# Optimization experiments

Hardware: AMD Instinct MI355X
Metric: run time of the kernel (lower is better)

Reference implementation:

```python
import jax, jax.numpy as jnp
import numpy as np

B, N, PATCH_DIM, HIDDEN, POS_SIZE = 16, 4096, 768, 768, 10240


def setup_inputs() -> dict:
    key = jax.random.key(0)
    k1, k2, k3, k4, k5 = jax.random.split(key, 5)
    pixel_values = jax.random.uniform(k1, (B, N, PATCH_DIM), dtype=jnp.float32)
    pixel_position_ids = jax.random.randint(k2, (B, N, 2), 0, POS_SIZE, dtype=jnp.int32)
    padding_mask = jax.random.randint(k3, (B, N), 0, 2).astype(bool)
    W_proj = jax.random.normal(k4, (HIDDEN, PATCH_DIM), dtype=jnp.float32) * 0.02
    pos_table = jax.random.normal(k5, (2, POS_SIZE, HIDDEN), dtype=jnp.float32) * 0.02
    return {
        "pixel_values": pixel_values,
        "pixel_position_ids": pixel_position_ids,
        "padding_mask": padding_mask,
        "W_proj": W_proj,
        "pos_table": pos_table,
    }


def reference(pixel_values, pixel_position_ids, padding_mask, W_proj, pos_table):
    # Rescale pixels to [-1, 1]
    x = 2.0 * (pixel_values - 0.5)
    # Linear(patch_dim -> hidden), bias=False: h = x @ W^T  -> [B, N, H]
    h = jnp.einsum("bnp,hp->bnh", x, W_proj)
    # Position embedding lookup. Original uses one_hot @ table; mathematically
    # identical to a direct gather per axis followed by a sum over the 2 axes.
    pos = jnp.clip(pixel_position_ids, 0, None)  # [B, N, 2]
    pe = pos_table[0][pos[..., 0]] + pos_table[1][pos[..., 1]]  # [B, N, H]
    pe = jnp.where(padding_mask[..., None], 0.0, pe)
    h = h + pe
    # masked_fill padded positions with 0
    h = jnp.where(padding_mask[..., None], 0.0, h)
    return h
```

## Files before the change

### kernel.cpp

```cpp
#include <hip/hip_runtime.h>
#include <hip/hip_bf16.h>

typedef __bf16 bf16_t;
typedef bf16_t bf16x4 __attribute__((ext_vector_type(4)));
typedef bf16_t bf16x8 __attribute__((ext_vector_type(8)));
typedef float f32x4 __attribute__((ext_vector_type(4)));

constexpr int NB   = 16;
constexpr int NN   = 4096;
constexpr int PD   = 768;
constexpr int HID  = 768;
constexpr int PSZ  = 10240;
constexpr int MT   = NB * NN;
constexpr int BM   = 128;
constexpr int BN   = 128;
constexpr int BK   = 32;
constexpr int NT   = PD / BK;
constexpr int LDSC = 132;
constexpr size_t PVN = (size_t)MT * PD;
constexpr size_t WN  = (size_t)HID * PD;

__device__ __forceinline__ bf16x8 cvt8_affine(const float4& x, const float4& y,
                                              float s, float o) {
    bf16x8 r;
    r[0] = (bf16_t)__builtin_fmaf(s, x.x, o);
    r[1] = (bf16_t)__builtin_fmaf(s, x.y, o);
    r[2] = (bf16_t)__builtin_fmaf(s, x.z, o);
    r[3] = (bf16_t)__builtin_fmaf(s, x.w, o);
    r[4] = (bf16_t)__builtin_fmaf(s, y.x, o);
    r[5] = (bf16_t)__builtin_fmaf(s, y.y, o);
    r[6] = (bf16_t)__builtin_fmaf(s, y.z, o);
    r[7] = (bf16_t)__builtin_fmaf(s, y.w, o);
    return r;
}

__device__ __forceinline__ bf16x4 cvt4_affine(const float4& x, float s, float o) {
    bf16x4 r;
    r[0] = (bf16_t)__builtin_fmaf(s, x.x, o);
    r[1] = (bf16_t)__builtin_fmaf(s, x.y, o);
    r[2] = (bf16_t)__builtin_fmaf(s, x.z, o);
    r[3] = (bf16_t)__builtin_fmaf(s, x.w, o);
    return r;
}

__global__ __launch_bounds__(256)
void compact_cvt(const float* __restrict__ pv,
                 const int* __restrict__ mask,
                 const float* __restrict__ W,
                 bf16_t* __restrict__ Ab,
                 bf16_t* __restrict__ Wb,
                 int* __restrict__ rowmap,
                 int* __restrict__ counter,
                 float* __restrict__ out)
{
    const int bid = blockIdx.x;
    const int tid = threadIdx.x;
    if (bid < 1024) {
        __shared__ int ls_slot[64];
        const int rowbase = bid * 64;
        const int lane = tid & 63;
        const int wv   = tid >> 6;
        if (wv == 0) {
            const int mk = mask[rowbase + lane];
            const unsigned long long b = __ballot(mk == 0);
            const int total = __popcll(b);
            const int pos = __popcll(b & ((1ull << lane) - 1ull));
            int gb = 0;
            if (lane == 0) gb = atomicAdd(counter, total);
            gb = __shfl(gb, 0);
            const int slot = (mk == 0) ? (gb + pos) : -1;
            ls_slot[lane] = slot;
            if (slot >= 0) rowmap[slot] = rowbase + lane;
        }
        __syncthreads();
        for (int i = wv; i < 64; i += 4) {
            const int slot = ls_slot[i];
            const int grow = rowbase + i;
            if (slot >= 0) {
                const float* src = pv + (size_t)grow * PD + lane * 12;
                bf16_t* dst = Ab + (size_t)slot * PD + lane * 12;
                #pragma unroll
                for (int q = 0; q < 3; ++q) {
                    const float4 v = *(const float4*)(src + q * 4);
                    *(bf16x4*)(dst + q * 4) = cvt4_affine(v, 2.f, -1.f);
                }
            } else {
                float* dst = out + (size_t)grow * HID + lane * 12;
                const float4 z{0.f, 0.f, 0.f, 0.f};
                #pragma unroll
                for (int q = 0; q < 3; ++q)
                    *(float4*)(dst + q * 4) = z;
            }
        }
    } else {
        const size_t nu = WN / 8;
        for (size_t u = (size_t)(bid - 1024) * 256 + tid; u < nu;
             u += (size_t)64 * 256) {
            const float4 x = ((const float4*)W)[2 * u];
            const float4 y = ((const float4*)W)[2 * u + 1];
            *(bf16x8*)(Wb + 8 * u) = cvt8_affine(x, y, 1.f, 0.f);
        }
    }
}

__global__ __launch_bounds__(256)
void cvt_kernel(const float* __restrict__ pv, const float* __restrict__ W,
                bf16_t* __restrict__ Ab, bf16_t* __restrict__ Wb)
{
    const size_t nunits = (PVN + WN) / 8;
    const size_t stride = (size_t)gridDim.x * blockDim.x;
    for (size_t u = (size_t)blockIdx.x * blockDim.x + threadIdx.x;
         u < nunits; u += stride) {
        if (u < PVN / 8) {
            const float4 x = ((const float4*)pv)[2 * u];
            const float4 y = ((const float4*)pv)[2 * u + 1];
            *(bf16x8*)(Ab + 8 * u) = cvt8_affine(x, y, 2.f, -1.f);
        } else {
            const size_t v = u - PVN / 8;
            const float4 x = ((const float4*)W)[2 * v];
            const float4 y = ((const float4*)W)[2 * v + 1];
            *(bf16x8*)(Wb + 8 * v) = cvt8_affine(x, y, 1.f, 0.f);
        }
    }
}

__device__ __forceinline__ void gload16(const void* g, void* l) {
    __builtin_amdgcn_global_load_lds(
        (const __attribute__((address_space(1))) void*)g,
        (__attribute__((address_space(3))) void*)l, 16, 0, 0);
}

template <bool USE_MAP>
__global__ __launch_bounds__(256, 2)
void gemm_kernel(const bf16_t* __restrict__ Ab,
                 const bf16_t* __restrict__ Wb,
                 const int* __restrict__ posids,
                 const int* __restrict__ mask,
                 const float* __restrict__ ptab,
                 float* __restrict__ out,
                 const int* __restrict__ rowmap,
                 const int* __restrict__ counter)
{
    __shared__ alignas(16) unsigned char smem[2 * (BM * BK + BN * BK) * 2];
    bf16_t* const Asb = (bf16_t*)smem;
    bf16_t* const Bsb = (bf16_t*)smem + 2 * BM * BK;
    float*  const Cs  = (float*)smem;

    int Mc = MT;
    int mt, nt;
    const int bid = blockIdx.x;
    if constexpr (USE_MAP) {
        Mc = counter[0];
        const int Mtiles = (Mc + BM - 1) / BM;
        const int nact = Mtiles * 6;
        if (bid >= nact) return;
        const int q = nact >> 3, rm = nact & 7;
        const int x = bid & 7, i = bid >> 3;
        const int logical = (x < rm ? x * (q + 1) : rm * (q + 1) + (x - rm) * q) + i;
        mt = logical / 6;
        nt = logical - mt * 6;
    } else {
        const int nwg = gridDim.x;
        const int cpx = nwg >> 3;
        const int logical = (bid & 7) * cpx + (bid >> 3);
        mt = logical / 6;
        nt = logical - mt * 6;
    }
    const int row0 = mt * BM;
    const int col0 = nt * BN;

    const int tid  = threadIdx.x;
    const int lane = tid & 63;
    const int wid  = tid >> 6;
    const int wm   = wid >> 1;
    const int wn   = wid & 1;

    const int srow = tid >> 2;
    const int sk   = (tid & 3) * 8;
    const bf16_t* a0 = Ab + (size_t)(row0 + srow) * PD + sk;
    const bf16_t* b0 = Wb + (size_t)(col0 + srow) * PD + sk;
    const int lds_lo = srow * BK + sk;
    const int lds_hi = (srow + 64) * BK + sk;

    f32x4 acc[4][4];
    #pragma unroll
    for (int i = 0; i < 4; ++i)
        #pragma unroll
        for (int j = 0; j < 4; ++j)
            acc[i][j] = f32x4{0.f, 0.f, 0.f, 0.f};

    const int lr = lane & 15;
    const int kg = lane >> 4;
    const int a_rd_off = (wm * 64 + lr) * BK + kg * 8;
    const int b_rd_off = (wn * 64 + lr) * BK + kg * 8;

    gload16(a0,           Asb + lds_lo);
    gload16(a0 + 64 * PD, Asb + lds_hi);
    gload16(b0,           Bsb + lds_lo);
    gload16(b0 + 64 * PD, Bsb + lds_hi);
    __syncthreads();

    int cur = 0;
    for (int t = 0; t < NT; ++t) {
        if (t + 1 < NT) {
            const int k1 = (t + 1) * BK;
            const int nb = cur ^ 1;
            gload16(a0 + k1,           Asb + nb * (BM * BK) + lds_lo);
            gload16(a0 + 64 * PD + k1, Asb + nb * (BM * BK) + lds_hi);
            gload16(b0 + k1,           Bsb + nb * (BN * BK) + lds_lo);
            gload16(b0 + 64 * PD + k1, Bsb + nb * (BN * BK) + lds_hi);
        }

        bf16x8 af[4], bfv[4];
        #pragma unroll
        for (int i = 0; i < 4; ++i) {
            af[i]  = *(const bf16x8*)(Asb + cur * (BM * BK) + a_rd_off + i * 16 * BK);
            bfv[i] = *(const bf16x8*)(Bsb + cur * (BN * BK) + b_rd_off + i * 16 * BK);
        }
        #pragma unroll
        for (int i = 0; i < 4; ++i)
            #pragma unroll
            for (int j = 0; j < 4; ++j)
                acc[i][j] = __builtin_amdgcn_mfma_f32_16x16x32_bf16(
                    af[i], bfv[j], acc[i][j], 0, 0, 0);

        __syncthreads();
        cur ^= 1;
    }

    const int lrow_w  = wm * 16 + kg * 4;
    const int lcol_w  = wn * 64 + lr;
    const int rr = tid >> 3;
    const int cg = tid & 7;
    const int erow_local = (rr & 15) + (rr >> 4) * 64;

    #pragma unroll
    for (int mi = 0; mi < 4; ++mi) {
        if (mi) __syncthreads();
        #pragma unroll
        for (int r = 0; r < 4; ++r)
            #pragma unroll
            for (int ni = 0; ni < 4; ++ni)
                Cs[(lrow_w + r) * LDSC + lcol_w + ni * 16] = acc[mi][ni][r];
        __syncthreads();

        const int crow = row0 + mi * 16 + erow_local;
        if constexpr (USE_MAP) {
            if (crow >= Mc) continue;
            const int grow = rowmap[crow];
            int p0 = posids[2 * grow];
            int p1 = posids[2 * grow + 1];
            p0 = p0 < 0 ? 0 : p0;
            p1 = p1 < 0 ? 0 : p1;
            const float* t0 = ptab + (size_t)p0 * HID + col0;
            const float* t1 = ptab + (size_t)PSZ * HID + (size_t)p1 * HID + col0;
            float* orow = out + (size_t)grow * HID + col0;
            #pragma unroll
            for (int j = 0; j < 4; ++j) {
                const int c = (cg + 8 * j) * 4;
                float4 v  = *(const float4*)&Cs[rr * LDSC + c];
                const float4 e0 = *(const float4*)(t0 + c);
                const float4 e1 = *(const float4*)(t1 + c);
                v.x += e0.x + e1.x;
                v.y += e0.y + e1.y;
                v.z += e0.z + e1.z;
                v.w += e0.w + e1.w;
                *(float4*)(orow + c) = v;
            }
        } else {
            const int grow = crow;
            float* orow = out + (size_t)grow * HID + col0;
            const int mk = mask[grow];
            if (mk) {
                const float4 z{0.f, 0.f, 0.f, 0.f};
                #pragma unroll
                for (int j = 0; j < 4; ++j)
                    *(float4*)(orow + (cg + 8 * j) * 4) = z;
            } else {
                int p0 = posids[2 * grow];
                int p1 = posids[2 * grow + 1];
                p0 = p0 < 0 ? 0 : p0;
                p1 = p1 < 0 ? 0 : p1;
                const float* t0 = ptab + (size_t)p0 * HID + col0;
                const float* t1 = ptab + (size_t)PSZ * HID + (size_t)p1 * HID + col0;
                #pragma unroll
                for (int j = 0; j < 4; ++j) {
                    const int c = (cg + 8 * j) * 4;
                    float4 v  = *(const float4*)&Cs[rr * LDSC + c];
                    const float4 e0 = *(const float4*)(t0 + c);
                    const float4 e1 = *(const float4*)(t1 + c);
                    v.x += e0.x + e1.x;
                    v.y += e0.y + e1.y;
                    v.z += e0.z + e1.z;
                    v.w += e0.w + e1.w;
                    *(float4*)(orow + c) = v;
                }
            }
        }
    }
}

constexpr int LDSS = 40;

__global__ __launch_bounds__(256, 2)
void vpe_kernel(const float* __restrict__ pv,
                const int* __restrict__ posids,
                const int* __restrict__ mask,
                const float* __restrict__ W,
                const float* __restrict__ ptab,
                float* __restrict__ out)
{
    __shared__ alignas(16) bf16_t As[2][BM * LDSS];
    __shared__ alignas(16) bf16_t Bs[2][BM * LDSS];

    const int nwg = gridDim.x;
    const int cpx = nwg >> 3;
    const int logical = (blockIdx.x & 7) * cpx + (blockIdx.x >> 3);
    const int mt = logical / 6;
    const int nt = logical - mt * 6;
    const int row0 = mt * BM;
    const int col0 = nt * BN;

    const int tid  = threadIdx.x;
    const int lane = tid & 63;
    const int wid  = tid >> 6;
    const int wm   = wid >> 1;
    const int wn   = wid & 1;
    const int srow = tid >> 1;
    const int scol = (tid & 1) << 4;

    const float* aptr = pv + (size_t)(row0 + srow) * PD + scol;
    const float* bptr = W  + (size_t)(col0 + srow) * PD + scol;
    const int lds_w_off = srow * LDSS + scol;

    f32x4 acc[4][4];
    #pragma unroll
    for (int i = 0; i < 4; ++i)
        #pragma unroll
        for (int j = 0; j < 4; ++j)
            acc[i][j] = f32x4{0.f, 0.f, 0.f, 0.f};

    const int lr = lane & 15;
    const int kg = lane >> 4;
    const int a_rd_off = (wm * 64 + lr) * LDSS + kg * 8;
    const int b_rd_off = (wn * 64 + lr) * LDSS + kg * 8;

    float4 ra[4], rb[4];
    #pragma unroll
    for (int q = 0; q < 4; ++q) {
        ra[q] = *(const float4*)(aptr + q * 4);
        rb[q] = *(const float4*)(bptr + q * 4);
    }
    {
        bf16x8 av0 = cvt8_affine(ra[0], ra[1], 2.f, -1.f);
        bf16x8 av1 = cvt8_affine(ra[2], ra[3], 2.f, -1.f);
        bf16x8 bv0 = cvt8_affine(rb[0], rb[1], 1.f, 0.f);
        bf16x8 bv1 = cvt8_affine(rb[2], rb[3], 1.f, 0.f);
        *(bf16x8*)(&As[0][lds_w_off])     = av0;
        *(bf16x8*)(&As[0][lds_w_off] + 8) = av1;
        *(bf16x8*)(&Bs[0][lds_w_off])     = bv0;
        *(bf16x8*)(&Bs[0][lds_w_off] + 8) = bv1;
    }
    __syncthreads();

    int cur = 0;
    for (int t = 0; t < NT - 1; ++t) {
        const int k1 = (t + 1) * BK;
        #pragma unroll
        for (int q = 0; q < 4; ++q) {
            ra[q] = *(const float4*)(aptr + k1 + q * 4);
            rb[q] = *(const float4*)(bptr + k1 + q * 4);
        }
        bf16x8 af[4], bfv[4];
        #pragma unroll
        for (int i = 0; i < 4; ++i) {
            af[i]  = *(const bf16x8*)(&As[cur][a_rd_off] + i * 16 * LDSS);
            bfv[i] = *(const bf16x8*)(&Bs[cur][b_rd_off] + i * 16 * LDSS);
        }
        #pragma unroll
        for (int i = 0; i < 4; ++i)
            #pragma unroll
            for (int j = 0; j < 4; ++j)
                acc[i][j] = __builtin_amdgcn_mfma_f32_16x16x32_bf16(
                    af[i], bfv[j], acc[i][j], 0, 0, 0);
        {
            bf16x8 av0 = cvt8_affine(ra[0], ra[1], 2.f, -1.f);
            bf16x8 av1 = cvt8_affine(ra[2], ra[3], 2.f, -1.f);
            bf16x8 bv0 = cvt8_affine(rb[0], rb[1], 1.f, 0.f);
            bf16x8 bv1 = cvt8_affine(rb[2], rb[3], 1.f, 0.f);
            const int nb = cur ^ 1;
            *(bf16x8*)(&As[nb][lds_w_off])     = av0;
            *(bf16x8*)(&As[nb][lds_w_off] + 8) = av1;
            *(bf16x8*)(&Bs[nb][lds_w_off])     = bv0;
            *(bf16x8*)(&Bs[nb][lds_w_off] + 8) = bv1;
        }
        __syncthreads();
        cur ^= 1;
    }
    {
        bf16x8 af[4], bfv[4];
        #pragma unroll
        for (int i = 0; i < 4; ++i) {
            af[i]  = *(const bf16x8*)(&As[cur][a_rd_off] + i * 16 * LDSS);
            bfv[i] = *(const bf16x8*)(&Bs[cur][b_rd_off] + i * 16 * LDSS);
        }
        #pragma unroll
        for (int i = 0; i < 4; ++i)
            #pragma unroll
            for (int j = 0; j < 4; ++j)
                acc[i][j] = __builtin_amdgcn_mfma_f32_16x16x32_bf16(
                    af[i], bfv[j], acc[i][j], 0, 0, 0);
    }
    #pragma unroll
    for (int mi = 0; mi < 4; ++mi) {
        #pragma unroll
        for (int r = 0; r < 4; ++r) {
            const int grow = row0 + wm * 64 + mi * 16 + kg * 4 + r;
            const int mk = mask[grow];
            int p0 = posids[2 * grow];
            int p1 = posids[2 * grow + 1];
            p0 = p0 < 0 ? 0 : p0;
            p1 = p1 < 0 ? 0 : p1;
            const float* t0 = ptab + (size_t)p0 * HID;
            const float* t1 = ptab + (size_t)PSZ * HID + (size_t)p1 * HID;
            float* orow = out + (size_t)grow * HID;
            #pragma unroll
            for (int ni = 0; ni < 4; ++ni) {
                const int col = col0 + wn * 64 + ni * 16 + lr;
                const float v = acc[mi][ni][r] + t0[col] + t1[col];
                orow[col] = mk ? 0.f : v;
            }
        }
    }
}

extern "C" void kernel_launch(void* const* d_in, const int* in_sizes, int n_in,
                              void* d_out, int out_size, void* d_ws, size_t ws_size,
                              hipStream_t stream) {
    (void)in_sizes; (void)n_in; (void)out_size;
    const float* pv     = (const float*)d_in[0];
    const int*   posids = (const int*)d_in[1];
    const int*   mask   = (const int*)d_in[2];
    const float* W      = (const float*)d_in[3];
    const float* ptab   = (const float*)d_in[4];
    float*       out    = (float*)d_out;

    const size_t AB_B = PVN * sizeof(bf16_t);
    const size_t WB_B = WN * sizeof(bf16_t);
    const size_t RM_B = (size_t)MT * 4;
    const size_t need1 = AB_B + WB_B;
    const size_t need2 = AB_B + WB_B + RM_B + 16;
    const int grid = (MT / BM) * (HID / BN);

    if (ws_size >= need2) {
        bf16_t* Ab   = (bf16_t*)d_ws;
        bf16_t* Wb   = Ab + PVN;
        int* rowmap  = (int*)((char*)d_ws + AB_B + WB_B);
        int* counter = (int*)((char*)d_ws + AB_B + WB_B + RM_B);
        hipMemsetAsync(counter, 0, 16, stream);
        hipLaunchKernelGGL(compact_cvt, dim3(1088), dim3(256), 0, stream,
                           pv, mask, W, Ab, Wb, rowmap, counter, out);
        hipLaunchKernelGGL((gemm_kernel<true>), dim3(grid), dim3(256), 0, stream,
                           Ab, Wb, posids, mask, ptab, out, rowmap, counter);
    } else if (ws_size >= need1) {
        bf16_t* Ab = (bf16_t*)d_ws;
        bf16_t* Wb = Ab + PVN;
        hipLaunchKernelGGL(cvt_kernel, dim3(2048), dim3(256), 0, stream,
                           pv, W, Ab, Wb);
        hipLaunchKernelGGL((gemm_kernel<false>), dim3(grid), dim3(256), 0, stream,
                           Ab, Wb, posids, mask, ptab, out, nullptr, nullptr);
    } else {
        hipLaunchKernelGGL(vpe_kernel, dim3(grid), dim3(256), 0, stream,
                           pv, posids, mask, W, ptab, out);
    }
}
```

Before: 167.6 us.

## Move masked-row zeroing into idle GEMM blocks and prefetch epilogue row indices

The compaction kernel now also records the indices of masked rows, stored from the end of rowmap, and no longer writes zeros to the output. GEMM blocks left idle by the compaction (beyond the active tile count) zero those masked output rows instead. This moves about half the output writes out of the conversion pass and overlaps them with the GEMM. The epilogue also loads each thread's rowmap and position ids for all four sub-tiles before the store loop, so that latency is not paid on every iteration. The cost is a second atomic per compaction block and a dependence on enough spare GEMM blocks existing.

```diff
diff --git a/kernel.cpp b/kernel.cpp
--- a/kernel.cpp
+++ b/kernel.cpp
@@ -50,8 +50,7 @@
                  bf16_t* __restrict__ Ab,
                  bf16_t* __restrict__ Wb,
                  int* __restrict__ rowmap,
-                 int* __restrict__ counter,
-                 float* __restrict__ out)
+                 int* __restrict__ counter)
 {
     const int bid = blockIdx.x;
     const int tid = threadIdx.x;
@@ -63,20 +62,32 @@
         if (wv == 0) {
             const int mk = mask[rowbase + lane];
             const unsigned long long b = __ballot(mk == 0);
+            const unsigned long long below = (1ull << lane) - 1ull;
             const int total = __popcll(b);
-            const int pos = __popcll(b & ((1ull << lane) - 1ull));
-            int gb = 0;
-            if (lane == 0) gb = atomicAdd(counter, total);
+            const int pos  = __popcll(b & below);
+            const int posm = __popcll(~b & below);
+            int gb = 0, gm = 0;
+            if (lane == 0) {
+                gb = atomicAdd(counter + 0, total);
+                gm = atomicAdd(counter + 1, 64 - total);
+            }
             gb = __shfl(gb, 0);
-            const int slot = (mk == 0) ? (gb + pos) : -1;
+            gm = __shfl(gm, 0);
+            int slot;
+            if (mk == 0) {
+                slot = gb + pos;
+                rowmap[slot] = rowbase + lane;
+            } else {
+                slot = -1;
+                rowmap[MT - 1 - (gm + posm)] = rowbase + lane;
+            }
             ls_slot[lane] = slot;
-            if (slot >= 0) rowmap[slot] = rowbase + lane;
         }
         __syncthreads();
         for (int i = wv; i < 64; i += 4) {
             const int slot = ls_slot[i];
-            const int grow = rowbase + i;
             if (slot >= 0) {
+                const int grow = rowbase + i;
                 const float* src = pv + (size_t)grow * PD + lane * 12;
                 bf16_t* dst = Ab + (size_t)slot * PD + lane * 12;
                 #pragma unroll
@@ -84,12 +95,6 @@
                     const float4 v = *(const float4*)(src + q * 4);
                     *(bf16x4*)(dst + q * 4) = cvt4_affine(v, 2.f, -1.f);
                 }
-            } else {
-                float* dst = out + (size_t)grow * HID + lane * 12;
-                const float4 z{0.f, 0.f, 0.f, 0.f};
-                #pragma unroll
-                for (int q = 0; q < 3; ++q)
-                    *(float4*)(dst + q * 4) = z;
             }
         }
     } else {
@@ -149,11 +154,27 @@
     int Mc = MT;
     int mt, nt;
     const int bid = blockIdx.x;
+    const int tid  = threadIdx.x;
+    const int lane = tid & 63;
+    const int wid  = tid >> 6;
     if constexpr (USE_MAP) {
         Mc = counter[0];
         const int Mtiles = (Mc + BM - 1) / BM;
         const int nact = Mtiles * 6;
-        if (bid >= nact) return;
+        if (bid >= nact) {
+            const int nspare = (int)gridDim.x - nact;
+            const int Mm = MT - Mc;
+            const int s = bid - nact;
+            const float4 z{0.f, 0.f, 0.f, 0.f};
+            for (int k = 4 * s + wid; k < Mm; k += 4 * nspare) {
+                const int grow = rowmap[MT - 1 - k];
+                float* dst = out + (size_t)grow * HID + lane * 12;
+                #pragma unroll
+                for (int q = 0; q < 3; ++q)
+                    *(float4*)(dst + q * 4) = z;
+            }
+            return;
+        }
         const int q = nact >> 3, rm = nact & 7;
         const int x = bid & 7, i = bid >> 3;
         const int logical = (x < rm ? x * (q + 1) : rm * (q + 1) + (x - rm) * q) + i;
@@ -169,9 +190,6 @@
     const int row0 = mt * BM;
     const int col0 = nt * BN;
 
-    const int tid  = threadIdx.x;
-    const int lane = tid & 63;
-    const int wid  = tid >> 6;
     const int wm   = wid >> 1;
     const int wn   = wid & 1;
 
@@ -234,6 +252,22 @@
     const int cg = tid & 7;
     const int erow_local = (rr & 15) + (rr >> 4) * 64;
 
+    int grow4[4], p04[4], p14[4];
+    #pragma unroll
+    for (int mi = 0; mi < 4; ++mi) {
+        int crow = row0 + mi * 16 + erow_local;
+        if constexpr (USE_MAP) {
+            const int cc = crow < Mc ? crow : Mc - 1;
+            grow4[mi] = rowmap[cc];
+        } else {
+            grow4[mi] = crow;
+        }
+        int p0 = posids[2 * grow4[mi]];
+        int p1 = posids[2 * grow4[mi] + 1];
+        p04[mi] = p0 < 0 ? 0 : p0;
+        p14[mi] = p1 < 0 ? 0 : p1;
+    }
+
     #pragma unroll
     for (int mi = 0; mi < 4; ++mi) {
         if (mi) __syncthreads();
@@ -247,14 +281,9 @@
         const int crow = row0 + mi * 16 + erow_local;
         if constexpr (USE_MAP) {
             if (crow >= Mc) continue;
-            const int grow = rowmap[crow];
-            int p0 = posids[2 * grow];
-            int p1 = posids[2 * grow + 1];
-            p0 = p0 < 0 ? 0 : p0;
-            p1 = p1 < 0 ? 0 : p1;
-            const float* t0 = ptab + (size_t)p0 * HID + col0;
-            const float* t1 = ptab + (size_t)PSZ * HID + (size_t)p1 * HID + col0;
-            float* orow = out + (size_t)grow * HID + col0;
+            const float* t0 = ptab + (size_t)p04[mi] * HID + col0;
+            const float* t1 = ptab + (size_t)PSZ * HID + (size_t)p14[mi] * HID + col0;
+            float* orow = out + (size_t)grow4[mi] * HID + col0;
             #pragma unroll
             for (int j = 0; j < 4; ++j) {
                 const int c = (cg + 8 * j) * 4;
@@ -277,12 +306,8 @@
                 for (int j = 0; j < 4; ++j)
                     *(float4*)(orow + (cg + 8 * j) * 4) = z;
             } else {
-                int p0 = posids[2 * grow];
-                int p1 = posids[2 * grow + 1];
-                p0 = p0 < 0 ? 0 : p0;
-                p1 = p1 < 0 ? 0 : p1;
-                const float* t0 = ptab + (size_t)p0 * HID + col0;
-                const float* t1 = ptab + (size_t)PSZ * HID + (size_t)p1 * HID + col0;
+                const float* t0 = ptab + (size_t)p04[mi] * HID + col0;
+                const float* t1 = ptab + (size_t)PSZ * HID + (size_t)p14[mi] * HID + col0;
                 #pragma unroll
                 for (int j = 0; j < 4; ++j) {
                     const int c = (cg + 8 * j) * 4;
@@ -459,7 +484,7 @@
         int* counter = (int*)((char*)d_ws + AB_B + WB_B + RM_B);
         hipMemsetAsync(counter, 0, 16, stream);
         hipLaunchKernelGGL(compact_cvt, dim3(1088), dim3(256), 0, stream,
-                           pv, mask, W, Ab, Wb, rowmap, counter, out);
+                           pv, mask, W, Ab, Wb, rowmap, counter);
         hipLaunchKernelGGL((gemm_kernel<true>), dim3(grid), dim3(256), 0, stream,
                            Ab, Wb, posids, mask, ptab, out, rowmap, counter);
     } else if (ws_size >= need1) {
```

Result: slower. 173.0 us (+3.2%).

## Load A fragments directly from global to registers, shrink LDS, raise occupancy

Applied to the files above, without the earlier changes.

The A operand is no longer staged through LDS. Each wave now loads its own bf16 fragments straight from global memory into registers every k-step, and only the W tile stays double-buffered in LDS. This shrinks shared memory enough to let launch bounds request four workgroups per CU instead of two. The epilogue also hoists the rowmap and position-id lookups ahead of the store loop. The risk is un-hidden global-load latency for A: those loads are issued in the same iteration they are consumed, there is no cross-wave reuse through LDS, and register pressure under the tighter launch bound may cause spills.

```diff
diff --git a/kernel.cpp b/kernel.cpp
--- a/kernel.cpp
+++ b/kernel.cpp
@@ -131,7 +131,7 @@
 }
 
 template <bool USE_MAP>
-__global__ __launch_bounds__(256, 2)
+__global__ __launch_bounds__(256, 4)
 void gemm_kernel(const bf16_t* __restrict__ Ab,
                  const bf16_t* __restrict__ Wb,
                  const int* __restrict__ posids,
@@ -141,9 +141,8 @@
                  const int* __restrict__ rowmap,
                  const int* __restrict__ counter)
 {
-    __shared__ alignas(16) unsigned char smem[2 * (BM * BK + BN * BK) * 2];
-    bf16_t* const Asb = (bf16_t*)smem;
-    bf16_t* const Bsb = (bf16_t*)smem + 2 * BM * BK;
+    __shared__ alignas(16) unsigned char smem[32 * LDSC * 4];
+    bf16_t* const Bsb = (bf16_t*)smem;
     float*  const Cs  = (float*)smem;
 
     int Mc = MT;
@@ -177,7 +176,6 @@
 
     const int srow = tid >> 2;
     const int sk   = (tid & 3) * 8;
-    const bf16_t* a0 = Ab + (size_t)(row0 + srow) * PD + sk;
     const bf16_t* b0 = Wb + (size_t)(col0 + srow) * PD + sk;
     const int lds_lo = srow * BK + sk;
     const int lds_hi = (srow + 64) * BK + sk;
@@ -191,32 +189,36 @@
 
     const int lr = lane & 15;
     const int kg = lane >> 4;
-    const int a_rd_off = (wm * 64 + lr) * BK + kg * 8;
     const int b_rd_off = (wn * 64 + lr) * BK + kg * 8;
 
-    gload16(a0,           Asb + lds_lo);
-    gload16(a0 + 64 * PD, Asb + lds_hi);
+    const bf16_t* aF[4];
+    #pragma unroll
+    for (int i = 0; i < 4; ++i)
+        aF[i] = Ab + (size_t)(row0 + wm * 64 + i * 16 + lr) * PD + kg * 8;
+
     gload16(b0,           Bsb + lds_lo);
     gload16(b0 + 64 * PD, Bsb + lds_hi);
     __syncthreads();
 
     int cur = 0;
     for (int t = 0; t < NT; ++t) {
+        bf16x8 af[4];
+        #pragma unroll
+        for (int i = 0; i < 4; ++i)
+            af[i] = *(const bf16x8*)(aF[i] + t * BK);
+
         if (t + 1 < NT) {
             const int k1 = (t + 1) * BK;
             const int nb = cur ^ 1;
-            gload16(a0 + k1,           Asb + nb * (BM * BK) + lds_lo);
-            gload16(a0 + 64 * PD + k1, Asb + nb * (BM * BK) + lds_hi);
             gload16(b0 + k1,           Bsb + nb * (BN * BK) + lds_lo);
             gload16(b0 + 64 * PD + k1, Bsb + nb * (BN * BK) + lds_hi);
         }
 
-        bf16x8 af[4], bfv[4];
-        #pragma unroll
-        for (int i = 0; i < 4; ++i) {
-            af[i]  = *(const bf16x8*)(Asb + cur * (BM * BK) + a_rd_off + i * 16 * BK);
+        bf16x8 bfv[4];
+        #pragma unroll
+        for (int i = 0; i < 4; ++i)
             bfv[i] = *(const bf16x8*)(Bsb + cur * (BN * BK) + b_rd_off + i * 16 * BK);
-        }
+
         #pragma unroll
         for (int i = 0; i < 4; ++i)
             #pragma unroll
@@ -234,9 +236,25 @@
     const int cg = tid & 7;
     const int erow_local = (rr & 15) + (rr >> 4) * 64;
 
+    int grow4[4], p04[4], p14[4];
     #pragma unroll
     for (int mi = 0; mi < 4; ++mi) {
-        if (mi) __syncthreads();
+        int crow = row0 + mi * 16 + erow_local;
+        if constexpr (USE_MAP) {
+            const int cc = crow < Mc ? crow : Mc - 1;
+            grow4[mi] = rowmap[cc];
+        } else {
+            grow4[mi] = crow;
+        }
+        int p0 = posids[2 * grow4[mi]];
+        int p1 = posids[2 * grow4[mi] + 1];
+        p04[mi] = p0 < 0 ? 0 : p0;
+        p14[mi] = p1 < 0 ? 0 : p1;
+    }
+
+    #pragma unroll
+    for (int mi = 0; mi < 4; ++mi) {
+        __syncthreads();
         #pragma unroll
         for (int r = 0; r < 4; ++r)
             #pragma unroll
@@ -247,14 +265,9 @@
         const int crow = row0 + mi * 16 + erow_local;
         if constexpr (USE_MAP) {
             if (crow >= Mc) continue;
-            const int grow = rowmap[crow];
-            int p0 = posids[2 * grow];
-            int p1 = posids[2 * grow + 1];
-            p0 = p0 < 0 ? 0 : p0;
-            p1 = p1 < 0 ? 0 : p1;
-            const float* t0 = ptab + (size_t)p0 * HID + col0;
-            const float* t1 = ptab + (size_t)PSZ * HID + (size_t)p1 * HID + col0;
-            float* orow = out + (size_t)grow * HID + col0;
+            const float* t0 = ptab + (size_t)p04[mi] * HID + col0;
+            const float* t1 = ptab + (size_t)PSZ * HID + (size_t)p14[mi] * HID + col0;
+            float* orow = out + (size_t)grow4[mi] * HID + col0;
             #pragma unroll
             for (int j = 0; j < 4; ++j) {
                 const int c = (cg + 8 * j) * 4;
@@ -277,12 +290,8 @@
                 for (int j = 0; j < 4; ++j)
                     *(float4*)(orow + (cg + 8 * j) * 4) = z;
             } else {
-                int p0 = posids[2 * grow];
-                int p1 = posids[2 * grow + 1];
-                p0 = p0 < 0 ? 0 : p0;
-                p1 = p1 < 0 ? 0 : p1;
-                const float* t0 = ptab + (size_t)p0 * HID + col0;
-                const float* t1 = ptab + (size_t)PSZ * HID + (size_t)p1 * HID + col0;
+                const float* t0 = ptab + (size_t)p04[mi] * HID + col0;
+                const float* t1 = ptab + (size_t)PSZ * HID + (size_t)p14[mi] * HID + col0;
                 #pragma unroll
                 for (int j = 0; j < 4; ++j) {
                     const int c = (cg + 8 * j) * 4;
```

New measurement: 208.6 us. 24.5% more time.
